# Kernel optimization log

Hardware: AMD Instinct MI355X
Metric: run time of the kernel (lower is better)

## Reference

```python
import jax, jax.numpy as jnp
import numpy as np

B, S, I, H, O, L = 64, 1024, 512, 512, 512, 3


def setup_inputs() -> dict:
    key = jax.random.key(0)
    ks = jax.random.split(key, 14)
    sc = 0.05  # small init to avoid gate saturation
    inp = {
        "input": jax.random.normal(ks[0], (B, S, I), jnp.float32),
        "hidden_state": jax.random.normal(ks[1], (B, L, H), jnp.float32),
        # gate params; x-side Linear has bias, h-side has none (as in torch module)
        "Wzx": jax.random.normal(ks[2], (L, I, H), jnp.float32) * sc,
        "bzx": jnp.zeros((L, H), jnp.float32),
        "Wzh": jax.random.normal(ks[3], (L, H, H), jnp.float32) * sc,
        "Wrx": jax.random.normal(ks[4], (L, I, H), jnp.float32) * sc,
        "brx": jnp.zeros((L, H), jnp.float32),
        "Wrh": jax.random.normal(ks[5], (L, H, H), jnp.float32) * sc,
        "Wgx": jax.random.normal(ks[6], (L, I, H), jnp.float32) * sc,
        "bgx": jnp.zeros((L, H), jnp.float32),
        "Wgh": jax.random.normal(ks[7], (L, H, H), jnp.float32) * sc,
        "Wout": jax.random.normal(ks[8], (H, O), jnp.float32) * sc,
        "bout": jnp.zeros((O,), jnp.float32),
    }
    return inp


def reference(input, hidden_state, Wzx, bzx, Wzh, Wrx, brx, Wrh, Wgx, bgx, Wgh, Wout, bout):
    n_layers = Wzx.shape[0]
    Bn = input.shape[0]
    Hn = hidden_state.shape[2]
    # layer_states: n_layers initial states + one extra zeros slot (matches torch code)
    states0 = jnp.concatenate(
        [jnp.transpose(hidden_state, (1, 0, 2)),
         jnp.zeros((1, Bn, Hn), input.dtype)], axis=0)  # (L+1, B, H)

    def step(states, x_t):
        x = x_t  # (B, I)
        for l in range(n_layers):
            # NOTE: faithfully reproduces the original's indexing: layer l reads
            # states[l], which for l>=1 was just overwritten by layer l-1 this step.
            h = states[l]
            z = jax.nn.sigmoid(x @ Wzx[l] + bzx[l] + h @ Wzh[l])
            r = jax.nn.sigmoid(x @ Wrx[l] + brx[l] + h @ Wrh[l])
            g = jnp.tanh(x @ Wgx[l] + bgx[l] + (r * h) @ Wgh[l])
            h = z * h + (1.0 - z) * g
            x = h  # dropout=0 -> identity
            states = states.at[l + 1].set(h)
        out_t = x @ Wout + bout  # (B, O)
        return states, out_t

    states_f, outs = jax.lax.scan(step, states0, jnp.transpose(input, (1, 0, 2)))
    layer_output = jnp.transpose(outs, (1, 0, 2))          # (B, S, O)
    hidden_out = jnp.transpose(states_f[:n_layers], (1, 0, 2))  # (B, L, H)
    return layer_output, hidden_out
```

## Files before the change

### kernel.cpp

```cpp
#include <hip/hip_runtime.h>


typedef __attribute__((ext_vector_type(4))) float f32x4;
typedef __attribute__((ext_vector_type(8))) __bf16 bf16x8;

#define NROWS 65536
#define HID_OFF 33554432ull

__device__ __forceinline__ void gload16(const void* g, void* l) {
  __builtin_amdgcn_global_load_lds((const __attribute__((address_space(1))) void*)g,
                                   (__attribute__((address_space(3))) void*)l,
                                   16, 0, 0);
}
__device__ __forceinline__ float sigmoidf_(float x) { return 1.f / (1.f + __expf(-x)); }
__device__ __forceinline__ float tanh_fast(float x) {
  const float e = __expf(2.f * x);
  return 1.f - 2.f / (e + 1.f);
}

__device__ __forceinline__ void stage32(const __bf16* __restrict__ src, int k0,
                                        __bf16* lds, int w, int lane) {
#pragma unroll
  for (int i = 0; i < 2; ++i) {
    const int s0 = (w * 2 + i) * 64;
    const int s = s0 + lane;
    const int row = s >> 2;
    const int cc = ((s & 3) ^ (row >> 1)) & 3;
    gload16(src + (size_t)row * 512 + k0 + cc * 8, lds + s0 * 8);
  }
}

__device__ __forceinline__ bf16x8 frag32(const __bf16* t, int row, int lane) {
  const int c = (((lane >> 4) ^ (row >> 1)) & 3);
  return *(const bf16x8*)(t + row * 32 + c * 8);
}

__device__ __forceinline__ void stage_ht(const __bf16* __restrict__ src,
                                         __bf16* Ht, int w, int lane) {
#pragma unroll
  for (int i = 0; i < 8; ++i) {
    const int s0 = i * 256 + w * 64;
    const int s = s0 + lane;
    const int row = s >> 4, cc = s & 15;
    gload16(src + (size_t)row * 512 + cc * 8, Ht + s0 * 8);
  }
  asm volatile("s_waitcnt vmcnt(0)");
  __builtin_amdgcn_sched_barrier(0);
  __builtin_amdgcn_s_barrier();
  __builtin_amdgcn_sched_barrier(0);
}

template<int EPI, bool L0>
__global__ __launch_bounds__(256, 4) void gemm12(
    const __bf16* __restrict__ A,
    const __bf16* __restrict__ Bt,
    int tiles_n, int row_off,
    const float* __restrict__ bias,
    const float* __restrict__ cterm,
    const float* __restrict__ h0f,
    const __bf16* __restrict__ haux,
    const __bf16* __restrict__ zf,
    const __bf16* __restrict__ gf,
    __bf16* __restrict__ o_rh,
    __bf16* __restrict__ o_h,
    float* __restrict__ o_f)
{
  __shared__ alignas(16) __bf16 smem[16384];
  __bf16* const A0 = smem;
  __bf16* const B0 = smem + 4096;
  __bf16* const A1 = smem + 8192;
  __bf16* const B1 = smem + 12288;

  const int tid = threadIdx.x, lane = tid & 63, w = tid >> 6;

  int bid = blockIdx.x;
  {
    const int nwg = gridDim.x;
    const int q = nwg >> 3, r = nwg & 7;
    const int x = bid & 7, rest = bid >> 3;
    bid = (x < r ? x * (q + 1) : r * (q + 1) + (x - r) * q) + rest;
  }
  const int tm = bid / tiles_n;
  const int tn = bid - tm * tiles_n;
  const size_t arow0 = (size_t)tm * 128;
  const int brow0 = tn * 128;
  const __bf16* const Ab = A + arow0 * 512;
  const __bf16* const Bb = Bt + (size_t)brow0 * 512;

  const int wr = (w >> 1) * 64;
  const int wc = (w & 1) * 64;

  f32x4 acc[4][4];
  const f32x4 zz = {0.f, 0.f, 0.f, 0.f};
#pragma unroll
  for (int i = 0; i < 4; ++i)
#pragma unroll
    for (int j = 0; j < 4; ++j) acc[i][j] = zz;

  auto stepf = [&](int t, const __bf16* cA, const __bf16* cB,
                   __bf16* nA, __bf16* nB) {
    if (t < 15) {
      stage32(Ab, (t + 1) * 32, nA, w, lane);
      stage32(Bb, (t + 1) * 32, nB, w, lane);
    }
    bf16x8 af[4], bb4[4];
#pragma unroll
    for (int i = 0; i < 4; ++i) {
      af[i]  = frag32(cA, wr + i * 16 + (lane & 15), lane);
      bb4[i] = frag32(cB, wc + i * 16 + (lane & 15), lane);
    }
#pragma unroll
    for (int mi = 0; mi < 4; ++mi)
#pragma unroll
      for (int ni = 0; ni < 4; ++ni)
        acc[mi][ni] = __builtin_amdgcn_mfma_f32_16x16x32_bf16(af[mi], bb4[ni], acc[mi][ni], 0, 0, 0);
    if (t < 15) {
      asm volatile("s_waitcnt vmcnt(0)");
      __builtin_amdgcn_sched_barrier(0);
    }
    __builtin_amdgcn_s_barrier();
    __builtin_amdgcn_sched_barrier(0);
  };

  stage32(Ab, 0, A0, w, lane);
  stage32(Bb, 0, B0, w, lane);
  asm volatile("s_waitcnt vmcnt(0)");
  __builtin_amdgcn_sched_barrier(0);
  __builtin_amdgcn_s_barrier();
  __builtin_amdgcn_sched_barrier(0);

#pragma unroll 1
  for (int t = 0; t < 16; t += 2) {
    stepf(t,     A0, B0, A1, B1);
    stepf(t + 1, A1, B1, A0, B0);
  }

  const int fcol = lane & 15;
  const int frow = (lane >> 4) * 4;
  const int bb0 = (row_off + (int)arow0) >> 10;

  if (EPI == 0) {
    if (tn < 4) {
      const size_t foff = ((size_t)(tm * 4 + tn)) * 16384 + (size_t)tid * 64;
      __bf16* zw = (__bf16*)zf;
#pragma unroll
      for (int mi = 0; mi < 4; ++mi) {
        bf16x8 p0, p1;
#pragma unroll
        for (int ni = 0; ni < 4; ++ni)
#pragma unroll
          for (int j = 0; j < 4; ++j) {
            const int gcol = brow0 + wc + ni * 16 + fcol;
            float c = acc[mi][ni][j] + bias[gcol];
            if (L0) c += cterm[bb0 * 1024 + gcol];
            const int idx = ni * 4 + j;
            if (idx < 8) p0[idx] = (__bf16)c; else p1[idx - 8] = (__bf16)c;
          }
        *(bf16x8*)(zw + foff + mi * 16) = p0;
        *(bf16x8*)(zw + foff + mi * 16 + 8) = p1;
      }
    } else if (tn < 8) {
      if (!L0) stage_ht(haux + arow0 * 512 + (tn - 4) * 128, smem, w, lane);
#pragma unroll
      for (int mi = 0; mi < 4; ++mi)
#pragma unroll
        for (int ni = 0; ni < 4; ++ni)
#pragma unroll
          for (int j = 0; j < 4; ++j) {
            const int rloc = (int)arow0 + wr + mi * 16 + frow + j;
            const int gcol = brow0 + wc + ni * 16 + fcol;
            const int nn = gcol - 512;
            float c = acc[mi][ni][j] + bias[gcol];
            if (L0) c += cterm[bb0 * 1024 + gcol];
            const float rv = sigmoidf_(c);
            const float h = L0 ? h0f[bb0 * 1536 + nn]
                               : (float)smem[(wr + mi * 16 + frow + j) * 128 + wc + ni * 16 + fcol];
            o_rh[(size_t)rloc * 512 + nn] = (__bf16)(rv * h);
          }
    } else {
      const size_t foff = ((size_t)(tm * 4 + (tn - 8))) * 16384 + (size_t)tid * 64;
      __bf16* gw = (__bf16*)gf;
#pragma unroll
      for (int mi = 0; mi < 4; ++mi) {
        bf16x8 p0, p1;
#pragma unroll
        for (int ni = 0; ni < 4; ++ni)
#pragma unroll
          for (int j = 0; j < 4; ++j) {
            const int gcol = brow0 + wc + ni * 16 + fcol;
            const float v = acc[mi][ni][j] + bias[gcol];
            const int idx = ni * 4 + j;
            if (idx < 8) p0[idx] = (__bf16)v; else p1[idx - 8] = (__bf16)v;
          }
        *(bf16x8*)(gw + foff + mi * 16) = p0;
        *(bf16x8*)(gw + foff + mi * 16 + 8) = p1;
      }
    }
  } else if (EPI == 1) {
    const size_t foff = ((size_t)(tm * 4 + tn)) * 16384 + (size_t)tid * 64;
    bf16x8 zr[4][2], gr[4][2];
#pragma unroll
    for (int mi = 0; mi < 4; ++mi) {
      zr[mi][0] = *(const bf16x8*)(zf + foff + mi * 16);
      zr[mi][1] = *(const bf16x8*)(zf + foff + mi * 16 + 8);
      gr[mi][0] = *(const bf16x8*)(gf + foff + mi * 16);
      gr[mi][1] = *(const bf16x8*)(gf + foff + mi * 16 + 8);
    }
    if (!L0) stage_ht(haux + arow0 * 512 + tn * 128, smem, w, lane);
    const bool has_last = (o_f != nullptr) && ((tm & 7) == 7);
#pragma unroll
    for (int mi = 0; mi < 4; ++mi) {
#pragma unroll
      for (int ni = 0; ni < 4; ++ni)
#pragma unroll
        for (int j = 0; j < 4; ++j) {
          const int rloc = (int)arow0 + wr + mi * 16 + frow + j;
          const int gcol = brow0 + wc + ni * 16 + fcol;
          const int idx = ni * 4 + j;
          const float zv = sigmoidf_((float)(idx < 8 ? zr[mi][0][idx] : zr[mi][1][idx - 8]));
          const float gp = (float)(idx < 8 ? gr[mi][0][idx] : gr[mi][1][idx - 8]);
          const float gv = tanh_fast(gp + acc[mi][ni][j]);
          const float h = L0 ? h0f[bb0 * 1536 + gcol]
                             : (float)smem[(wr + mi * 16 + frow + j) * 128 + wc + ni * 16 + fcol];
          const float hv = zv * h + (1.f - zv) * gv;
          o_h[(size_t)rloc * 512 + gcol] = (__bf16)hv;
          if (has_last && ((rloc & 1023) == 1023))
            o_f[(size_t)bb0 * 1536 + gcol] = (float)(__bf16)hv;
        }
    }
  } else {
#pragma unroll
    for (int mi = 0; mi < 4; ++mi)
#pragma unroll
      for (int ni = 0; ni < 4; ++ni)
#pragma unroll
        for (int j = 0; j < 4; ++j) {
          const int rloc = (int)arow0 + wr + mi * 16 + frow + j;
          const int gcol = brow0 + wc + ni * 16 + fcol;
          o_f[(size_t)rloc * 512 + gcol] = acc[mi][ni][j] + bias[gcol];
        }
  }
}


__global__ void prep_pack(const float* __restrict__ Wzx, const float* __restrict__ Wzh,
                          const float* __restrict__ Wrx, const float* __restrict__ Wrh,
                          const float* __restrict__ Wgx, const float* __restrict__ Wgh,
                          const float* __restrict__ Wout,
                          __bf16* __restrict__ W1t, __bf16* __restrict__ Wght,
                          __bf16* __restrict__ Woutt)
{
  const int slot = blockIdx.z;
  const float* srcA;
  const float* srcB = nullptr;
  __bf16* dst;
  if (slot < 9) {
    const int l = slot / 3, g = slot % 3;
    srcA = (g == 0 ? Wzx : g == 1 ? Wrx : Wgx) + (size_t)l * 512 * 512;
    if (l > 0 && g < 2) srcB = (g == 0 ? Wzh : Wrh) + (size_t)l * 512 * 512;
    dst = W1t + (size_t)l * 1536 * 512 + (size_t)g * 512 * 512;
  } else if (slot < 12) {
    const int l = slot - 9;
    srcA = Wgh + (size_t)l * 512 * 512;
    dst = Wght + (size_t)l * 512 * 512;
  } else {
    srcA = Wout;
    dst = Woutt;
  }
  __shared__ float tile[32][33];
  const int k0 = blockIdx.x * 32;
  const int n0 = blockIdx.y * 32;
  const int tx = threadIdx.x;
  const int ty = threadIdx.y;
  for (int i = ty; i < 32; i += 8) {
    float v = srcA[(size_t)(k0 + i) * 512 + n0 + tx];
    if (srcB) v += srcB[(size_t)(k0 + i) * 512 + n0 + tx];
    tile[i][tx] = v;
  }
  __syncthreads();
  for (int i = ty; i < 32; i += 8)
    dst[(size_t)(n0 + i) * 512 + k0 + tx] = (__bf16)tile[tx][i];
}

__global__ void cterm_kernel(const float* __restrict__ hidden,
                             const float* __restrict__ Wzh,
                             const float* __restrict__ Wrh,
                             float* __restrict__ Cterm)
{
  const int idx = blockIdx.x * blockDim.x + threadIdx.x;
  const int b = idx >> 10;
  const int n = idx & 1023;
  const float* W = (n < 512 ? Wzh : Wrh);
  const int nn = n & 511;
  const float* h0 = hidden + (size_t)b * 1536;
  float acc = 0.f;
  for (int k = 0; k < 512; ++k) acc += h0[k] * W[(size_t)k * 512 + nn];
  Cterm[idx] = acc;
}

__global__ void small_prep(const float* __restrict__ bzx, const float* __restrict__ brx,
                           const float* __restrict__ bgx, const float* __restrict__ hidden,
                           float* __restrict__ bias1, float* __restrict__ out_hidden)
{
  const int idx = blockIdx.x * blockDim.x + threadIdx.x;
  if (idx < 3 * 1536) {
    const int l = idx / 1536, j = idx % 1536;
    const float* src = (j < 512 ? bzx : j < 1024 ? brx : bgx);
    bias1[idx] = src[l * 512 + (j & 511)];
  }
  const int hidx = idx - 3 * 1536;
  if (hidx >= 0 && hidx < 64 * 512) {
    const int b = hidx >> 9, n = hidx & 511;
    out_hidden[(size_t)b * 1536 + n] = hidden[(size_t)b * 1536 + n];
  }
}

__global__ void convert_x(const float* __restrict__ src, __bf16* __restrict__ dst, long n)
{
  const long i = ((long)blockIdx.x * blockDim.x + threadIdx.x) * 8;
  if (i >= n) return;
  const f32x4 a = *(const f32x4*)(src + i);
  const f32x4 b = *(const f32x4*)(src + i + 4);
  bf16x8 o;
  o[0] = (__bf16)a[0]; o[1] = (__bf16)a[1]; o[2] = (__bf16)a[2]; o[3] = (__bf16)a[3];
  o[4] = (__bf16)b[0]; o[5] = (__bf16)b[1]; o[6] = (__bf16)b[2]; o[7] = (__bf16)b[3];
  *(bf16x8*)(dst + i) = o;
}

extern "C" void kernel_launch(void* const* d_in, const int* in_sizes, int n_in,
                              void* d_out, int out_size, void* d_ws, size_t ws_size,
                              hipStream_t stream) {
  const float* input  = (const float*)d_in[0];
  const float* hidden = (const float*)d_in[1];
  const float* Wzx = (const float*)d_in[2];
  const float* bzx = (const float*)d_in[3];
  const float* Wzh = (const float*)d_in[4];
  const float* Wrx = (const float*)d_in[5];
  const float* brx = (const float*)d_in[6];
  const float* Wrh = (const float*)d_in[7];
  const float* Wgx = (const float*)d_in[8];
  const float* bgx = (const float*)d_in[9];
  const float* Wgh = (const float*)d_in[10];
  const float* Wout = (const float*)d_in[11];
  const float* bout = (const float*)d_in[12];

  float* out = (float*)d_out;
  float* out_hidden = out + HID_OFF;

  char* ws = (char*)d_ws;
  size_t off = 0;
  auto carve = [&](size_t bytes) -> void* {
    off = (off + 255) & ~(size_t)255;
    void* p = ws + off;
    off += bytes;
    return p;
  };

  __bf16* W1t   = (__bf16*)carve(3ull * 1536 * 512 * 2);
  __bf16* Wght  = (__bf16*)carve(3ull * 512 * 512 * 2);
  __bf16* Woutt = (__bf16*)carve(512ull * 512 * 2);
  float*  bias1 = (float*) carve(3ull * 1536 * 4);
  float*  Cterm = (float*) carve(64ull * 1024 * 4);
  const size_t fixed_end = off;

  long chunk_rows = NROWS;
  int C = 1;
  while (C < 32) {
    const size_t need = ((fixed_end + 255) & ~(size_t)255) +
                        5ull * (size_t)chunk_rows * 512 * 2 + 5 * 256;
    if (need <= ws_size) break;
    C *= 2;
    chunk_rows /= 2;
  }
  __bf16* bufA  = (__bf16*)carve((size_t)chunk_rows * 512 * 2);
  __bf16* bufB  = (__bf16*)carve((size_t)chunk_rows * 512 * 2);
  __bf16* zfrag = (__bf16*)carve((size_t)chunk_rows * 512 * 2);
  __bf16* rhb   = (__bf16*)carve((size_t)chunk_rows * 512 * 2);
  __bf16* gfrag = (__bf16*)carve((size_t)chunk_rows * 512 * 2);

  small_prep<<<(3 * 1536 + 64 * 512 + 255) / 256, 256, 0, stream>>>(
      bzx, brx, bgx, hidden, bias1, out_hidden);
  dim3 tp_grid(16, 16, 13), tp_blk(32, 8);
  prep_pack<<<tp_grid, tp_blk, 0, stream>>>(Wzx, Wzh, Wrx, Wrh, Wgx, Wgh, Wout,
                                            W1t, Wght, Woutt);
  cterm_kernel<<<65536 / 256, 256, 0, stream>>>(hidden, Wzh, Wrh, Cterm);

  for (int c = 0; c < C; ++c) {
    const long row_off = (long)c * chunk_rows;
    const long nelem = chunk_rows * 512;
    const int mt = (int)(chunk_rows / 128);

    convert_x<<<(int)((nelem / 8 + 255) / 256), 256, 0, stream>>>(
        input + (size_t)row_off * 512, bufA, nelem);

    gemm12<0, true><<<mt * 12, 256, 0, stream>>>(
        bufA, W1t, 12, (int)row_off, bias1, Cterm, hidden, nullptr,
        zfrag, gfrag, rhb, nullptr, nullptr);
    gemm12<1, true><<<mt * 4, 256, 0, stream>>>(
        rhb, Wght, 4, (int)row_off, nullptr, nullptr, hidden, nullptr,
        zfrag, gfrag, nullptr, bufB, out_hidden + 512);

    gemm12<0, false><<<mt * 12, 256, 0, stream>>>(
        bufB, W1t + 1536 * 512, 12, (int)row_off, bias1 + 1536, nullptr, nullptr, bufB,
        zfrag, gfrag, rhb, nullptr, nullptr);
    gemm12<1, false><<<mt * 4, 256, 0, stream>>>(
        rhb, Wght + 512 * 512, 4, (int)row_off, nullptr, nullptr, nullptr, bufB,
        zfrag, gfrag, nullptr, bufA, out_hidden + 1024);

    gemm12<0, false><<<mt * 12, 256, 0, stream>>>(
        bufA, W1t + 2 * 1536 * 512, 12, (int)row_off, bias1 + 3072, nullptr, nullptr, bufA,
        zfrag, gfrag, rhb, nullptr, nullptr);
    gemm12<1, false><<<mt * 4, 256, 0, stream>>>(
        rhb, Wght + 2 * 512 * 512, 4, (int)row_off, nullptr, nullptr, nullptr, bufA,
        zfrag, gfrag, nullptr, bufB, nullptr);

    gemm12<2, false><<<mt * 4, 256, 0, stream>>>(
        bufB, Woutt, 4, (int)row_off, bout, nullptr, nullptr, nullptr,
        nullptr, nullptr, nullptr, nullptr, out + (size_t)row_off * 512);
  }
}
```

Before: 931.8 us.

## Load MFMA fragments directly from global memory into registers, dropping LDS staging

The GEMM main loop no longer stages A/B tiles through swizzled LDS with barriers. Each lane loads its bf16x8 MFMA fragments straight from global memory into double-buffered registers, and launch bounds drop to 3 waves per SIMD to make room. The z-gate sigmoid also moves from the second GEMM's epilogue into the first GEMM's epilogue, before the bf16 store. This removes LDS traffic and the per-step barriers, but gives up the cross-wave sharing of tiles, so A/B rows are re-read per wave and the kernel depends on L1/L2 hits and more registers.

```diff
diff --git a/kernel.cpp b/kernel.cpp
--- a/kernel.cpp
+++ b/kernel.cpp
@@ -16,23 +16,6 @@
 __device__ __forceinline__ float tanh_fast(float x) {
   const float e = __expf(2.f * x);
   return 1.f - 2.f / (e + 1.f);
-}
-
-__device__ __forceinline__ void stage32(const __bf16* __restrict__ src, int k0,
-                                        __bf16* lds, int w, int lane) {
-#pragma unroll
-  for (int i = 0; i < 2; ++i) {
-    const int s0 = (w * 2 + i) * 64;
-    const int s = s0 + lane;
-    const int row = s >> 2;
-    const int cc = ((s & 3) ^ (row >> 1)) & 3;
-    gload16(src + (size_t)row * 512 + k0 + cc * 8, lds + s0 * 8);
-  }
-}
-
-__device__ __forceinline__ bf16x8 frag32(const __bf16* t, int row, int lane) {
-  const int c = (((lane >> 4) ^ (row >> 1)) & 3);
-  return *(const bf16x8*)(t + row * 32 + c * 8);
 }
 
 __device__ __forceinline__ void stage_ht(const __bf16* __restrict__ src,
@@ -51,7 +34,7 @@
 }
 
 template<int EPI, bool L0>
-__global__ __launch_bounds__(256, 4) void gemm12(
+__global__ __launch_bounds__(256, 3) void gemm13(
     const __bf16* __restrict__ A,
     const __bf16* __restrict__ Bt,
     int tiles_n, int row_off,
@@ -66,10 +49,6 @@
     float* __restrict__ o_f)
 {
   __shared__ alignas(16) __bf16 smem[16384];
-  __bf16* const A0 = smem;
-  __bf16* const B0 = smem + 4096;
-  __bf16* const A1 = smem + 8192;
-  __bf16* const B1 = smem + 12288;
 
   const int tid = threadIdx.x, lane = tid & 63, w = tid >> 6;
 
@@ -84,12 +63,13 @@
   const int tn = bid - tm * tiles_n;
   const size_t arow0 = (size_t)tm * 128;
   const int brow0 = tn * 128;
-  const __bf16* const Ab = A + arow0 * 512;
-  const __bf16* const Bb = Bt + (size_t)brow0 * 512;
 
   const int wr = (w >> 1) * 64;
   const int wc = (w & 1) * 64;
 
+  const __bf16* const Ap = A  + (arow0 + wr + (lane & 15)) * 512 + (lane >> 4) * 8;
+  const __bf16* const Bp = Bt + ((size_t)brow0 + wc + (lane & 15)) * 512 + (lane >> 4) * 8;
+
   f32x4 acc[4][4];
   const f32x4 zz = {0.f, 0.f, 0.f, 0.f};
 #pragma unroll
@@ -97,42 +77,30 @@
 #pragma unroll
     for (int j = 0; j < 4; ++j) acc[i][j] = zz;
 
-  auto stepf = [&](int t, const __bf16* cA, const __bf16* cB,
-                   __bf16* nA, __bf16* nB) {
-    if (t < 15) {
-      stage32(Ab, (t + 1) * 32, nA, w, lane);
-      stage32(Bb, (t + 1) * 32, nB, w, lane);
+  bf16x8 a0[4], b0[4], a1[4], b1[4];
+
+  auto ldfrag = [&](int t, bf16x8 (&fa)[4], bf16x8 (&fb)[4]) {
+#pragma unroll
+    for (int i = 0; i < 4; ++i) {
+      fa[i] = *(const bf16x8*)(Ap + i * 8192 + t * 32);
+      fb[i] = *(const bf16x8*)(Bp + i * 8192 + t * 32);
     }
-    bf16x8 af[4], bb4[4];
-#pragma unroll
-    for (int i = 0; i < 4; ++i) {
-      af[i]  = frag32(cA, wr + i * 16 + (lane & 15), lane);
-      bb4[i] = frag32(cB, wc + i * 16 + (lane & 15), lane);
-    }
+  };
+  auto domfma = [&](bf16x8 (&fa)[4], bf16x8 (&fb)[4]) {
 #pragma unroll
     for (int mi = 0; mi < 4; ++mi)
 #pragma unroll
       for (int ni = 0; ni < 4; ++ni)
-        acc[mi][ni] = __builtin_amdgcn_mfma_f32_16x16x32_bf16(af[mi], bb4[ni], acc[mi][ni], 0, 0, 0);
-    if (t < 15) {
-      asm volatile("s_waitcnt vmcnt(0)");
-      __builtin_amdgcn_sched_barrier(0);
-    }
-    __builtin_amdgcn_s_barrier();
-    __builtin_amdgcn_sched_barrier(0);
+        acc[mi][ni] = __builtin_amdgcn_mfma_f32_16x16x32_bf16(fa[mi], fb[ni], acc[mi][ni], 0, 0, 0);
   };
 
-  stage32(Ab, 0, A0, w, lane);
-  stage32(Bb, 0, B0, w, lane);
-  asm volatile("s_waitcnt vmcnt(0)");
-  __builtin_amdgcn_sched_barrier(0);
-  __builtin_amdgcn_s_barrier();
-  __builtin_amdgcn_sched_barrier(0);
-
+  ldfrag(0, a0, b0);
 #pragma unroll 1
   for (int t = 0; t < 16; t += 2) {
-    stepf(t,     A0, B0, A1, B1);
-    stepf(t + 1, A1, B1, A0, B0);
+    ldfrag(t + 1, a1, b1);
+    domfma(a0, b0);
+    if (t + 2 < 16) ldfrag(t + 2, a0, b0);
+    domfma(a1, b1);
   }
 
   const int fcol = lane & 15;
@@ -153,8 +121,9 @@
             const int gcol = brow0 + wc + ni * 16 + fcol;
             float c = acc[mi][ni][j] + bias[gcol];
             if (L0) c += cterm[bb0 * 1024 + gcol];
+            const float v = sigmoidf_(c);
             const int idx = ni * 4 + j;
-            if (idx < 8) p0[idx] = (__bf16)c; else p1[idx - 8] = (__bf16)c;
+            if (idx < 8) p0[idx] = (__bf16)v; else p1[idx - 8] = (__bf16)v;
           }
         *(bf16x8*)(zw + foff + mi * 16) = p0;
         *(bf16x8*)(zw + foff + mi * 16 + 8) = p1;
@@ -217,7 +186,7 @@
           const int rloc = (int)arow0 + wr + mi * 16 + frow + j;
           const int gcol = brow0 + wc + ni * 16 + fcol;
           const int idx = ni * 4 + j;
-          const float zv = sigmoidf_((float)(idx < 8 ? zr[mi][0][idx] : zr[mi][1][idx - 8]));
+          const float zv = (float)(idx < 8 ? zr[mi][0][idx] : zr[mi][1][idx - 8]);
           const float gp = (float)(idx < 8 ? gr[mi][0][idx] : gr[mi][1][idx - 8]);
           const float gv = tanh_fast(gp + acc[mi][ni][j]);
           const float h = L0 ? h0f[bb0 * 1536 + gcol]
@@ -393,28 +362,28 @@
     convert_x<<<(int)((nelem / 8 + 255) / 256), 256, 0, stream>>>(
         input + (size_t)row_off * 512, bufA, nelem);
 
-    gemm12<0, true><<<mt * 12, 256, 0, stream>>>(
+    gemm13<0, true><<<mt * 12, 256, 0, stream>>>(
         bufA, W1t, 12, (int)row_off, bias1, Cterm, hidden, nullptr,
         zfrag, gfrag, rhb, nullptr, nullptr);
-    gemm12<1, true><<<mt * 4, 256, 0, stream>>>(
+    gemm13<1, true><<<mt * 4, 256, 0, stream>>>(
         rhb, Wght, 4, (int)row_off, nullptr, nullptr, hidden, nullptr,
         zfrag, gfrag, nullptr, bufB, out_hidden + 512);
 
-    gemm12<0, false><<<mt * 12, 256, 0, stream>>>(
+    gemm13<0, false><<<mt * 12, 256, 0, stream>>>(
         bufB, W1t + 1536 * 512, 12, (int)row_off, bias1 + 1536, nullptr, nullptr, bufB,
         zfrag, gfrag, rhb, nullptr, nullptr);
-    gemm12<1, false><<<mt * 4, 256, 0, stream>>>(
+    gemm13<1, false><<<mt * 4, 256, 0, stream>>>(
         rhb, Wght + 512 * 512, 4, (int)row_off, nullptr, nullptr, nullptr, bufB,
         zfrag, gfrag, nullptr, bufA, out_hidden + 1024);
 
-    gemm12<0, false><<<mt * 12, 256, 0, stream>>>(
+    gemm13<0, false><<<mt * 12, 256, 0, stream>>>(
         bufA, W1t + 2 * 1536 * 512, 12, (int)row_off, bias1 + 3072, nullptr, nullptr, bufA,
         zfrag, gfrag, rhb, nullptr, nullptr);
-    gemm12<1, false><<<mt * 4, 256, 0, stream>>>(
+    gemm13<1, false><<<mt * 4, 256, 0, stream>>>(
         rhb, Wght + 2 * 512 * 512, 4, (int)row_off, nullptr, nullptr, nullptr, bufA,
         zfrag, gfrag, nullptr, bufB, nullptr);
 
-    gemm12<2, false><<<mt * 4, 256, 0, stream>>>(
+    gemm13<2, false><<<mt * 4, 256, 0, stream>>>(
         bufB, Woutt, 4, (int)row_off, bout, nullptr, nullptr, nullptr,
         nullptr, nullptr, nullptr, nullptr, out + (size_t)row_off * 512);
   }
```

Measured after the change: 1.798 ms. 1.93x slower.

## Load B fragments directly to registers and precompute z sigmoid in first GEMM

Applied to the files above, without the earlier changes.

The GEMM no longer stages the weight (B) tile through LDS. Each lane loads its B fragments straight from global memory into double-buffered registers, and waits with vmcnt(4) so the prefetch can overlap the MFMAs. The z-gate sigmoid moves into the first GEMM's epilogue, so the second GEMM reads stored sigmoid values, and launch bounds drop to 3 waves-per-EU to leave room for the extra registers. The direct loads are uncoalesced 16-byte strided reads whose reuse now depends on L1/L2 instead of LDS. Storing z as bf16 after the sigmoid slightly changes rounding, and the LDS array is still declared at its old size even though half of it is now unused.

```diff
diff --git a/kernel.cpp b/kernel.cpp
--- a/kernel.cpp
+++ b/kernel.cpp
@@ -51,7 +51,7 @@
 }
 
 template<int EPI, bool L0>
-__global__ __launch_bounds__(256, 4) void gemm12(
+__global__ __launch_bounds__(256, 3) void gemm18(
     const __bf16* __restrict__ A,
     const __bf16* __restrict__ Bt,
     int tiles_n, int row_off,
@@ -67,9 +67,7 @@
 {
   __shared__ alignas(16) __bf16 smem[16384];
   __bf16* const A0 = smem;
-  __bf16* const B0 = smem + 4096;
-  __bf16* const A1 = smem + 8192;
-  __bf16* const B1 = smem + 12288;
+  __bf16* const A1 = smem + 4096;
 
   const int tid = threadIdx.x, lane = tid & 63, w = tid >> 6;
 
@@ -85,11 +83,12 @@
   const size_t arow0 = (size_t)tm * 128;
   const int brow0 = tn * 128;
   const __bf16* const Ab = A + arow0 * 512;
-  const __bf16* const Bb = Bt + (size_t)brow0 * 512;
 
   const int wr = (w >> 1) * 64;
   const int wc = (w & 1) * 64;
 
+  const __bf16* const Bp = Bt + ((size_t)brow0 + wc + (lane & 15)) * 512 + (lane >> 4) * 8;
+
   f32x4 acc[4][4];
   const f32x4 zz = {0.f, 0.f, 0.f, 0.f};
 #pragma unroll
@@ -97,25 +96,31 @@
 #pragma unroll
     for (int j = 0; j < 4; ++j) acc[i][j] = zz;
 
-  auto stepf = [&](int t, const __bf16* cA, const __bf16* cB,
-                   __bf16* nA, __bf16* nB) {
+  bf16x8 bf0[4], bf1[4];
+
+  auto ldB = [&](int t, bf16x8 (&bf)[4]) {
+#pragma unroll
+    for (int i = 0; i < 4; ++i)
+      bf[i] = *(const bf16x8*)(Bp + (size_t)i * 16 * 512 + t * 32);
+  };
+
+  auto stepf = [&](int t, const __bf16* cA, __bf16* nA,
+                   bf16x8 (&bfN)[4], bf16x8 (&bfC)[4]) {
     if (t < 15) {
       stage32(Ab, (t + 1) * 32, nA, w, lane);
-      stage32(Bb, (t + 1) * 32, nB, w, lane);
+      ldB(t + 1, bfN);
     }
-    bf16x8 af[4], bb4[4];
-#pragma unroll
-    for (int i = 0; i < 4; ++i) {
-      af[i]  = frag32(cA, wr + i * 16 + (lane & 15), lane);
-      bb4[i] = frag32(cB, wc + i * 16 + (lane & 15), lane);
-    }
+    bf16x8 af[4];
+#pragma unroll
+    for (int i = 0; i < 4; ++i)
+      af[i] = frag32(cA, wr + i * 16 + (lane & 15), lane);
 #pragma unroll
     for (int mi = 0; mi < 4; ++mi)
 #pragma unroll
       for (int ni = 0; ni < 4; ++ni)
-        acc[mi][ni] = __builtin_amdgcn_mfma_f32_16x16x32_bf16(af[mi], bb4[ni], acc[mi][ni], 0, 0, 0);
+        acc[mi][ni] = __builtin_amdgcn_mfma_f32_16x16x32_bf16(af[mi], bfC[ni], acc[mi][ni], 0, 0, 0);
     if (t < 15) {
-      asm volatile("s_waitcnt vmcnt(0)");
+      asm volatile("s_waitcnt vmcnt(4)");
       __builtin_amdgcn_sched_barrier(0);
     }
     __builtin_amdgcn_s_barrier();
@@ -123,16 +128,16 @@
   };
 
   stage32(Ab, 0, A0, w, lane);
-  stage32(Bb, 0, B0, w, lane);
-  asm volatile("s_waitcnt vmcnt(0)");
+  ldB(0, bf0);
+  asm volatile("s_waitcnt vmcnt(4)");
   __builtin_amdgcn_sched_barrier(0);
   __builtin_amdgcn_s_barrier();
   __builtin_amdgcn_sched_barrier(0);
 
 #pragma unroll 1
   for (int t = 0; t < 16; t += 2) {
-    stepf(t,     A0, B0, A1, B1);
-    stepf(t + 1, A1, B1, A0, B0);
+    stepf(t,     A0, A1, bf1, bf0);
+    stepf(t + 1, A1, A0, bf0, bf1);
   }
 
   const int fcol = lane & 15;
@@ -153,8 +158,9 @@
             const int gcol = brow0 + wc + ni * 16 + fcol;
             float c = acc[mi][ni][j] + bias[gcol];
             if (L0) c += cterm[bb0 * 1024 + gcol];
+            const float v = sigmoidf_(c);
             const int idx = ni * 4 + j;
-            if (idx < 8) p0[idx] = (__bf16)c; else p1[idx - 8] = (__bf16)c;
+            if (idx < 8) p0[idx] = (__bf16)v; else p1[idx - 8] = (__bf16)v;
           }
         *(bf16x8*)(zw + foff + mi * 16) = p0;
         *(bf16x8*)(zw + foff + mi * 16 + 8) = p1;
@@ -217,7 +223,7 @@
           const int rloc = (int)arow0 + wr + mi * 16 + frow + j;
           const int gcol = brow0 + wc + ni * 16 + fcol;
           const int idx = ni * 4 + j;
-          const float zv = sigmoidf_((float)(idx < 8 ? zr[mi][0][idx] : zr[mi][1][idx - 8]));
+          const float zv = (float)(idx < 8 ? zr[mi][0][idx] : zr[mi][1][idx - 8]);
           const float gp = (float)(idx < 8 ? gr[mi][0][idx] : gr[mi][1][idx - 8]);
           const float gv = tanh_fast(gp + acc[mi][ni][j]);
           const float h = L0 ? h0f[bb0 * 1536 + gcol]
@@ -393,28 +399,28 @@
     convert_x<<<(int)((nelem / 8 + 255) / 256), 256, 0, stream>>>(
         input + (size_t)row_off * 512, bufA, nelem);
 
-    gemm12<0, true><<<mt * 12, 256, 0, stream>>>(
+    gemm18<0, true><<<mt * 12, 256, 0, stream>>>(
         bufA, W1t, 12, (int)row_off, bias1, Cterm, hidden, nullptr,
         zfrag, gfrag, rhb, nullptr, nullptr);
-    gemm12<1, true><<<mt * 4, 256, 0, stream>>>(
+    gemm18<1, true><<<mt * 4, 256, 0, stream>>>(
         rhb, Wght, 4, (int)row_off, nullptr, nullptr, hidden, nullptr,
         zfrag, gfrag, nullptr, bufB, out_hidden + 512);
 
-    gemm12<0, false><<<mt * 12, 256, 0, stream>>>(
+    gemm18<0, false><<<mt * 12, 256, 0, stream>>>(
         bufB, W1t + 1536 * 512, 12, (int)row_off, bias1 + 1536, nullptr, nullptr, bufB,
         zfrag, gfrag, rhb, nullptr, nullptr);
-    gemm12<1, false><<<mt * 4, 256, 0, stream>>>(
+    gemm18<1, false><<<mt * 4, 256, 0, stream>>>(
         rhb, Wght + 512 * 512, 4, (int)row_off, nullptr, nullptr, nullptr, bufB,
         zfrag, gfrag, nullptr, bufA, out_hidden + 1024);
 
-    gemm12<0, false><<<mt * 12, 256, 0, stream>>>(
+    gemm18<0, false><<<mt * 12, 256, 0, stream>>>(
         bufA, W1t + 2 * 1536 * 512, 12, (int)row_off, bias1 + 3072, nullptr, nullptr, bufA,
         zfrag, gfrag, rhb, nullptr, nullptr);
-    gemm12<1, false><<<mt * 4, 256, 0, stream>>>(
+    gemm18<1, false><<<mt * 4, 256, 0, stream>>>(
         rhb, Wght + 2 * 512 * 512, 4, (int)row_off, nullptr, nullptr, nullptr, bufA,
         zfrag, gfrag, nullptr, bufB, nullptr);
 
-    gemm12<2, false><<<mt * 4, 256, 0, stream>>>(
+    gemm18<2, false><<<mt * 4, 256, 0, stream>>>(
         bufB, Woutt, 4, (int)row_off, bout, nullptr, nullptr, nullptr,
         nullptr, nullptr, nullptr, nullptr, out + (size_t)row_off * 512);
   }
```

After: 1.280 ms. 37.3% more time.
